# Optimization experiments

Hardware: AMD Instinct MI355X
Metric: run time of the kernel (lower is better)

Reference implementation:

```python
import jax, jax.numpy as jnp
import numpy as np

INPUT_DIM = 512
HIDDEN_DIM = 512
T, B = 512, 128


def setup_inputs() -> dict:
    key = jax.random.key(0)
    ks = jax.random.split(key, 9)
    s_in = 1.0 / np.sqrt(INPUT_DIM + HIDDEN_DIM)
    d = INPUT_DIM + HIDDEN_DIM
    inputs = jax.random.normal(ks[0], (T, B, INPUT_DIM), dtype=jnp.float32)
    def lin(kw, kb):
        W = jax.random.uniform(kw, (HIDDEN_DIM, d), minval=-s_in, maxval=s_in, dtype=jnp.float32)
        b = jax.random.uniform(kb, (HIDDEN_DIM,), minval=-s_in, maxval=s_in, dtype=jnp.float32)
        return W, b
    Wf, bf = lin(ks[1], ks[2])
    Wi, bi = lin(ks[3], ks[4])
    Wg, bg = lin(ks[5], ks[6])
    Wo, bo = lin(ks[7], ks[8])
    return {"inputs": inputs, "Wf": Wf, "bf": bf, "Wi": Wi, "bi": bi,
            "Wg": Wg, "bg": bg, "Wo": Wo, "bo": bo}


def _lstm(inputs, Wf, bf, Wi, bi, Wg, bg, Wo, bo):
    B_ = inputs.shape[1]
    h0 = jnp.zeros((B_, HIDDEN_DIM), dtype=inputs.dtype)
    c0 = jnp.zeros((B_, HIDDEN_DIM), dtype=inputs.dtype)

    def step(carry, x):
        hx, cx = carry
        combined = jnp.concatenate([x, hx], axis=1)  # [B, input+hidden]
        f = jax.nn.sigmoid(combined @ Wf.T + bf)
        i = jax.nn.sigmoid(combined @ Wi.T + bi)
        g = jnp.tanh(combined @ Wg.T + bg)
        o = jax.nn.sigmoid(combined @ Wo.T + bo)
        cx = f * cx + i * g
        hx = o * jnp.tanh(cx)
        return (hx, cx), hx

    (hx, cx), outputs = jax.lax.scan(step, (h0, c0), inputs)
    return outputs, (hx, cx)


def reference(inputs, Wf, bf, Wi, bi, Wg, bg, Wo, bo):
    return _lstm(inputs, Wf, bf, Wi, bi, Wg, bg, Wo, bo)
```

## Files before the change

kernel.cpp:

```cpp
#include <hip/hip_runtime.h>
#include <stdint.h>

#define T_STEPS 512
#define BATCH   128
#define HID     512
#define KTOT    1024

typedef __attribute__((ext_vector_type(8))) short          bf16x8;
typedef __attribute__((ext_vector_type(8))) unsigned short u16x8;
typedef __attribute__((ext_vector_type(4))) float          f32x4;

__device__ inline unsigned short f2bf(float f) {
    union { float f; unsigned u; } x; x.f = f;
    unsigned r = x.u + 0x7FFFu + ((x.u >> 16) & 1u);
    return (unsigned short)(r >> 16);
}

__device__ inline float sigmoidf_(float x) { return 1.f / (1.f + __expf(-x)); }
__device__ inline float tanhf_(float x)    { float e = __expf(2.f * x); return 1.f - 2.f / (e + 1.f); }

__global__ void cast_x_kernel(const float* __restrict__ x, unsigned short* __restrict__ y, int n) {
    int i = (blockIdx.x * blockDim.x + threadIdx.x) * 8;
    if (i >= n) return;
    float4 a = *(const float4*)(x + i);
    float4 b = *(const float4*)(x + i + 4);
    u16x8 v;
    v[0] = f2bf(a.x); v[1] = f2bf(a.y); v[2] = f2bf(a.z); v[3] = f2bf(a.w);
    v[4] = f2bf(b.x); v[5] = f2bf(b.y); v[6] = f2bf(b.z); v[7] = f2bf(b.w);
    *(u16x8*)(y + i) = v;
}

__global__ __launch_bounds__(512, 2) void lstm_kernel(
    const float* __restrict__ xf,
    const unsigned short* __restrict__ xbf,
    const float* __restrict__ Wf, const float* __restrict__ bfv,
    const float* __restrict__ Wi, const float* __restrict__ biv,
    const float* __restrict__ Wg, const float* __restrict__ bgv,
    const float* __restrict__ Wo, const float* __restrict__ bov,
    float* __restrict__ out,
    unsigned int* __restrict__ flags,
    unsigned short* __restrict__ hbuf,
    int use_xbf)
{
    __shared__ __align__(16) unsigned short comb[16][1048];
    __shared__ float gatesl[4][16][33];
    __shared__ float cl[16][33];

    const int tid  = threadIdx.x;
    const int bgc  = blockIdx.x >> 4;
    const int cg   = blockIdx.x & 15;
    const int w    = tid >> 6;
    const int lane = tid & 63;
    const int gate = w & 3;
    const int uh   = w >> 2;
    const int n    = lane & 15;
    const int quad = lane >> 4;
    const int unit = cg * 32 + uh * 16 + n;

    const float* Wp = (gate == 0) ? Wf : (gate == 1) ? Wi : (gate == 2) ? Wg : Wo;
    const float* bp = (gate == 0) ? bfv : (gate == 1) ? biv : (gate == 2) ? bgv : bov;
    const float bias = bp[unit];

    bf16x8 wfr[32];
    const float* wrow = Wp + (size_t)unit * KTOT;
#pragma unroll
    for (int kk = 0; kk < 32; ++kk) {
        const float4* p = (const float4*)(wrow + kk * 32 + quad * 8);
        float4 a = p[0], b = p[1];
        u16x8 v;
        v[0] = f2bf(a.x); v[1] = f2bf(a.y); v[2] = f2bf(a.z); v[3] = f2bf(a.w);
        v[4] = f2bf(b.x); v[5] = f2bf(b.y); v[6] = f2bf(b.z); v[7] = f2bf(b.w);
        wfr[kk] = (bf16x8)v;
    }

    {
        const int b = tid >> 5, u = tid & 31;
        cl[b][u] = 0.f;
    }

    const int srow = tid >> 5;
    const int scol = tid & 31;

    for (int t = 0; t < T_STEPS; ++t) {
        if (use_xbf) {
            const uint4* src = (const uint4*)(xbf + ((size_t)(t * BATCH + bgc * 16 + srow)) * HID + scol * 16);
            uint4 v0 = src[0], v1 = src[1];
            *(uint4*)&comb[srow][scol * 16]     = v0;
            *(uint4*)&comb[srow][scol * 16 + 8] = v1;
        } else {
            const float4* src = (const float4*)(xf + ((size_t)(t * BATCH + bgc * 16 + srow)) * HID + scol * 16);
            float4 a0 = src[0], a1 = src[1], a2 = src[2], a3 = src[3];
            u16x8 v;
            v[0] = f2bf(a0.x); v[1] = f2bf(a0.y); v[2] = f2bf(a0.z); v[3] = f2bf(a0.w);
            v[4] = f2bf(a1.x); v[5] = f2bf(a1.y); v[6] = f2bf(a1.z); v[7] = f2bf(a1.w);
            *(u16x8*)&comb[srow][scol * 16] = v;
            u16x8 v2;
            v2[0] = f2bf(a2.x); v2[1] = f2bf(a2.y); v2[2] = f2bf(a2.z); v2[3] = f2bf(a2.w);
            v2[4] = f2bf(a3.x); v2[5] = f2bf(a3.y); v2[6] = f2bf(a3.z); v2[7] = f2bf(a3.w);
            *(u16x8*)&comb[srow][scol * 16 + 8] = v2;
        }
        __syncthreads();

        f32x4 acc0a = {0.f, 0.f, 0.f, 0.f}, acc0b = {0.f, 0.f, 0.f, 0.f};
#pragma unroll
        for (int kk = 0; kk < 16; kk += 2) {
            bf16x8 a0 = *(const bf16x8*)&comb[n][kk * 32 + quad * 8];
            bf16x8 a1 = *(const bf16x8*)&comb[n][(kk + 1) * 32 + quad * 8];
            acc0a = __builtin_amdgcn_mfma_f32_16x16x32_bf16(a0, wfr[kk],     acc0a, 0, 0, 0);
            acc0b = __builtin_amdgcn_mfma_f32_16x16x32_bf16(a1, wfr[kk + 1], acc0b, 0, 0, 0);
        }

        if (t > 0) {
            if (tid < 16) {
                unsigned int* fp = flags + ((size_t)(t - 1) * 8 + bgc) * 16 + tid;
                while (__hip_atomic_load(fp, __ATOMIC_RELAXED, __HIP_MEMORY_SCOPE_AGENT) == 0u) {
                    __builtin_amdgcn_s_sleep(1);
                }
            }
            __syncthreads();
            const unsigned long long* src = (const unsigned long long*)
                (hbuf + (size_t)((t - 1) & 1) * BATCH * HID + (size_t)(bgc * 16 + srow) * HID + scol * 16);
            unsigned long long v0 = __hip_atomic_load(src + 0, __ATOMIC_RELAXED, __HIP_MEMORY_SCOPE_AGENT);
            unsigned long long v1 = __hip_atomic_load(src + 1, __ATOMIC_RELAXED, __HIP_MEMORY_SCOPE_AGENT);
            unsigned long long v2 = __hip_atomic_load(src + 2, __ATOMIC_RELAXED, __HIP_MEMORY_SCOPE_AGENT);
            unsigned long long v3 = __hip_atomic_load(src + 3, __ATOMIC_RELAXED, __HIP_MEMORY_SCOPE_AGENT);
            unsigned long long* dst = (unsigned long long*)&comb[srow][512 + scol * 16];
            dst[0] = v0; dst[1] = v1; dst[2] = v2; dst[3] = v3;
        } else {
            uint4 z = {0u, 0u, 0u, 0u};
            *(uint4*)&comb[srow][512 + scol * 16]     = z;
            *(uint4*)&comb[srow][512 + scol * 16 + 8] = z;
        }
        __syncthreads();

        f32x4 acc1a = {0.f, 0.f, 0.f, 0.f}, acc1b = {0.f, 0.f, 0.f, 0.f};
#pragma unroll
        for (int kk = 16; kk < 32; kk += 2) {
            bf16x8 a0 = *(const bf16x8*)&comb[n][kk * 32 + quad * 8];
            bf16x8 a1 = *(const bf16x8*)&comb[n][(kk + 1) * 32 + quad * 8];
            acc1a = __builtin_amdgcn_mfma_f32_16x16x32_bf16(a0, wfr[kk],     acc1a, 0, 0, 0);
            acc1b = __builtin_amdgcn_mfma_f32_16x16x32_bf16(a1, wfr[kk + 1], acc1b, 0, 0, 0);
        }

#pragma unroll
        for (int r = 0; r < 4; ++r) {
            float v = acc0a[r] + acc0b[r] + acc1a[r] + acc1b[r] + bias;
            v = (gate == 2) ? tanhf_(v) : sigmoidf_(v);
            gatesl[gate][quad * 4 + r][uh * 16 + n] = v;
        }
        __syncthreads();

        {
            const int b = tid >> 5, u = tid & 31;
            float fv = gatesl[0][b][u], iv = gatesl[1][b][u];
            float gv = gatesl[2][b][u], ov = gatesl[3][b][u];
            float cn = fv * cl[b][u] + iv * gv;
            cl[b][u] = cn;
            float hv = ov * tanhf_(cn);
            const int bglob = bgc * 16 + b;
            const int uglob = cg * 32 + u;
            out[(size_t)t * BATCH * HID + (size_t)bglob * HID + uglob] = hv;
            if (t == T_STEPS - 1) {
                out[(size_t)T_STEPS * BATCH * HID + (size_t)bglob * HID + uglob] = hv;
                out[(size_t)T_STEPS * BATCH * HID + BATCH * HID + (size_t)bglob * HID + uglob] = cn;
            }
            unsigned int us  = (unsigned int)f2bf(hv);
            unsigned int us1 = (unsigned int)__shfl_down((int)us, 1);
            if ((u & 1) == 0) {
                unsigned int pv = us | (us1 << 16);
                unsigned int* hp = (unsigned int*)(hbuf + (size_t)(t & 1) * BATCH * HID
                                                   + (size_t)bglob * HID + uglob);
                __hip_atomic_store(hp, pv, __ATOMIC_RELAXED, __HIP_MEMORY_SCOPE_AGENT);
            }
        }
        __builtin_amdgcn_s_waitcnt(0);
        __syncthreads();
        if (tid == 0) {
            __hip_atomic_store(flags + ((size_t)t * 8 + bgc) * 16 + cg, 1u,
                               __ATOMIC_RELAXED, __HIP_MEMORY_SCOPE_AGENT);
        }
    }
}

extern "C" void kernel_launch(void* const* d_in, const int* in_sizes, int n_in,
                              void* d_out, int out_size, void* d_ws, size_t ws_size,
                              hipStream_t stream) {
    (void)in_sizes; (void)n_in; (void)out_size;
    const float* x   = (const float*)d_in[0];
    const float* Wf  = (const float*)d_in[1];
    const float* bfv = (const float*)d_in[2];
    const float* Wi  = (const float*)d_in[3];
    const float* biv = (const float*)d_in[4];
    const float* Wg  = (const float*)d_in[5];
    const float* bgv = (const float*)d_in[6];
    const float* Wo  = (const float*)d_in[7];
    const float* bov = (const float*)d_in[8];
    float* out = (float*)d_out;

    unsigned char* ws = (unsigned char*)d_ws;
    unsigned int*   flags = (unsigned int*)ws;
    unsigned short* hbuf  = (unsigned short*)(ws + 262144);
    unsigned short* xbf   = (unsigned short*)(ws + 524288);

    size_t need = 524288 + (size_t)T_STEPS * BATCH * HID * 2;
    int use_xbf = (ws_size >= need) ? 1 : 0;

    hipMemsetAsync(flags, 0, 262144, stream);
    if (use_xbf) {
        int nelem = T_STEPS * BATCH * HID;
        cast_x_kernel<<<nelem / (256 * 8), 256, 0, stream>>>(x, xbf, nelem);
    }
    lstm_kernel<<<dim3(128), dim3(512), 0, stream>>>(
        x, xbf, Wf, bfv, Wi, biv, Wg, bgv, Wo, bov, out, flags, hbuf, use_xbf);
}
```

Before: 1.971 ms.

## Software-pipeline input projection and prefetch x ahead of the recurrent wait

Restructures the time loop so the input half of the gate GEMM for step t+1 is computed right after step t's gate math. The next x tile is prefetched two steps ahead into registers and written to shared memory early, so global load latency and the x-part MFMAs sit off the wait for the hidden state. The cell state moves from shared memory into a per-thread register. Every wave now spins on the flags itself without sleeping, which removes one block barrier but adds polling traffic. The x-part MFMAs now run before the step's completion flag is published, which may lengthen the cross-block critical path.

```diff
diff --git a/kernel.cpp b/kernel.cpp
--- a/kernel.cpp
+++ b/kernel.cpp
@@ -28,6 +28,25 @@
     v[0] = f2bf(a.x); v[1] = f2bf(a.y); v[2] = f2bf(a.z); v[3] = f2bf(a.w);
     v[4] = f2bf(b.x); v[5] = f2bf(b.y); v[6] = f2bf(b.z); v[7] = f2bf(b.w);
     *(u16x8*)(y + i) = v;
+}
+
+__device__ inline void load_x32(const float* xf, const unsigned short* xbf, int use_xbf,
+                                size_t off, uint4& a, uint4& b) {
+    if (use_xbf) {
+        const uint4* p = (const uint4*)(xbf + off);
+        a = p[0]; b = p[1];
+    } else {
+        const float4* p = (const float4*)(xf + off);
+        float4 f0 = p[0], f1 = p[1], f2 = p[2], f3 = p[3];
+        u16x8 v;
+        v[0] = f2bf(f0.x); v[1] = f2bf(f0.y); v[2] = f2bf(f0.z); v[3] = f2bf(f0.w);
+        v[4] = f2bf(f1.x); v[5] = f2bf(f1.y); v[6] = f2bf(f1.z); v[7] = f2bf(f1.w);
+        a = *(uint4*)&v;
+        u16x8 w;
+        w[0] = f2bf(f2.x); w[1] = f2bf(f2.y); w[2] = f2bf(f2.z); w[3] = f2bf(f2.w);
+        w[4] = f2bf(f3.x); w[5] = f2bf(f3.y); w[6] = f2bf(f3.z); w[7] = f2bf(f3.w);
+        b = *(uint4*)&w;
+    }
 }
 
 __global__ __launch_bounds__(512, 2) void lstm_kernel(
@@ -44,7 +63,6 @@
 {
     __shared__ __align__(16) unsigned short comb[16][1048];
     __shared__ float gatesl[4][16][33];
-    __shared__ float cl[16][33];
 
     const int tid  = threadIdx.x;
     const int bgc  = blockIdx.x >> 4;
@@ -73,111 +91,123 @@
         wfr[kk] = (bf16x8)v;
     }
 
-    {
-        const int b = tid >> 5, u = tid & 31;
-        cl[b][u] = 0.f;
-    }
-
     const int srow = tid >> 5;
     const int scol = tid & 31;
 
+    const int bc = srow, uc = scol;
+    float creg = 0.f;
+    const int bglob = bgc * 16 + bc;
+    const int uglob = cg * 32 + uc;
+
+    const size_t xstride = (size_t)HID;
+
+    {
+        uint4 a, b;
+        load_x32(xf, xbf, use_xbf, ((size_t)(0 * BATCH + bgc * 16 + srow)) * xstride + scol * 16, a, b);
+        *(uint4*)&comb[srow][scol * 16]     = a;
+        *(uint4*)&comb[srow][scol * 16 + 8] = b;
+        uint4 z = {0u, 0u, 0u, 0u};
+        *(uint4*)&comb[srow][512 + scol * 16]     = z;
+        *(uint4*)&comb[srow][512 + scol * 16 + 8] = z;
+    }
+    __syncthreads();
+
+    f32x4 axa = {0.f, 0.f, 0.f, 0.f}, axb = {0.f, 0.f, 0.f, 0.f};
+#pragma unroll
+    for (int kk = 0; kk < 16; kk += 2) {
+        bf16x8 a0 = *(const bf16x8*)&comb[n][kk * 32 + quad * 8];
+        bf16x8 a1 = *(const bf16x8*)&comb[n][(kk + 1) * 32 + quad * 8];
+        axa = __builtin_amdgcn_mfma_f32_16x16x32_bf16(a0, wfr[kk],     axa, 0, 0, 0);
+        axb = __builtin_amdgcn_mfma_f32_16x16x32_bf16(a1, wfr[kk + 1], axb, 0, 0, 0);
+    }
+
+    uint4 pfa, pfb;
+    load_x32(xf, xbf, use_xbf, ((size_t)(1 * BATCH + bgc * 16 + srow)) * xstride + scol * 16, pfa, pfb);
+
     for (int t = 0; t < T_STEPS; ++t) {
-        if (use_xbf) {
-            const uint4* src = (const uint4*)(xbf + ((size_t)(t * BATCH + bgc * 16 + srow)) * HID + scol * 16);
-            uint4 v0 = src[0], v1 = src[1];
-            *(uint4*)&comb[srow][scol * 16]     = v0;
-            *(uint4*)&comb[srow][scol * 16 + 8] = v1;
-        } else {
-            const float4* src = (const float4*)(xf + ((size_t)(t * BATCH + bgc * 16 + srow)) * HID + scol * 16);
-            float4 a0 = src[0], a1 = src[1], a2 = src[2], a3 = src[3];
-            u16x8 v;
-            v[0] = f2bf(a0.x); v[1] = f2bf(a0.y); v[2] = f2bf(a0.z); v[3] = f2bf(a0.w);
-            v[4] = f2bf(a1.x); v[5] = f2bf(a1.y); v[6] = f2bf(a1.z); v[7] = f2bf(a1.w);
-            *(u16x8*)&comb[srow][scol * 16] = v;
-            u16x8 v2;
-            v2[0] = f2bf(a2.x); v2[1] = f2bf(a2.y); v2[2] = f2bf(a2.z); v2[3] = f2bf(a2.w);
-            v2[4] = f2bf(a3.x); v2[5] = f2bf(a3.y); v2[6] = f2bf(a3.z); v2[7] = f2bf(a3.w);
-            *(u16x8*)&comb[srow][scol * 16 + 8] = v2;
-        }
-        __syncthreads();
-
-        f32x4 acc0a = {0.f, 0.f, 0.f, 0.f}, acc0b = {0.f, 0.f, 0.f, 0.f};
-#pragma unroll
-        for (int kk = 0; kk < 16; kk += 2) {
-            bf16x8 a0 = *(const bf16x8*)&comb[n][kk * 32 + quad * 8];
-            bf16x8 a1 = *(const bf16x8*)&comb[n][(kk + 1) * 32 + quad * 8];
-            acc0a = __builtin_amdgcn_mfma_f32_16x16x32_bf16(a0, wfr[kk],     acc0a, 0, 0, 0);
-            acc0b = __builtin_amdgcn_mfma_f32_16x16x32_bf16(a1, wfr[kk + 1], acc0b, 0, 0, 0);
-        }
-
         if (t > 0) {
-            if (tid < 16) {
-                unsigned int* fp = flags + ((size_t)(t - 1) * 8 + bgc) * 16 + tid;
-                while (__hip_atomic_load(fp, __ATOMIC_RELAXED, __HIP_MEMORY_SCOPE_AGENT) == 0u) {
-                    __builtin_amdgcn_s_sleep(1);
-                }
-            }
-            __syncthreads();
+            if (lane < 16) {
+                unsigned int* fp = flags + ((size_t)(t - 1) * 8 + bgc) * 16 + lane;
+                while (__hip_atomic_load(fp, __ATOMIC_RELAXED, __HIP_MEMORY_SCOPE_AGENT) == 0u) {}
+            }
             const unsigned long long* src = (const unsigned long long*)
                 (hbuf + (size_t)((t - 1) & 1) * BATCH * HID + (size_t)(bgc * 16 + srow) * HID + scol * 16);
             unsigned long long v0 = __hip_atomic_load(src + 0, __ATOMIC_RELAXED, __HIP_MEMORY_SCOPE_AGENT);
             unsigned long long v1 = __hip_atomic_load(src + 1, __ATOMIC_RELAXED, __HIP_MEMORY_SCOPE_AGENT);
             unsigned long long v2 = __hip_atomic_load(src + 2, __ATOMIC_RELAXED, __HIP_MEMORY_SCOPE_AGENT);
             unsigned long long v3 = __hip_atomic_load(src + 3, __ATOMIC_RELAXED, __HIP_MEMORY_SCOPE_AGENT);
-            unsigned long long* dst = (unsigned long long*)&comb[srow][512 + scol * 16];
-            dst[0] = v0; dst[1] = v1; dst[2] = v2; dst[3] = v3;
-        } else {
-            uint4 z = {0u, 0u, 0u, 0u};
-            *(uint4*)&comb[srow][512 + scol * 16]     = z;
-            *(uint4*)&comb[srow][512 + scol * 16 + 8] = z;
+            uint4 a, b;
+            a.x = (unsigned)v0; a.y = (unsigned)(v0 >> 32);
+            a.z = (unsigned)v1; a.w = (unsigned)(v1 >> 32);
+            b.x = (unsigned)v2; b.y = (unsigned)(v2 >> 32);
+            b.z = (unsigned)v3; b.w = (unsigned)(v3 >> 32);
+            *(uint4*)&comb[srow][512 + scol * 16]     = a;
+            *(uint4*)&comb[srow][512 + scol * 16 + 8] = b;
         }
         __syncthreads();
 
-        f32x4 acc1a = {0.f, 0.f, 0.f, 0.f}, acc1b = {0.f, 0.f, 0.f, 0.f};
 #pragma unroll
         for (int kk = 16; kk < 32; kk += 2) {
             bf16x8 a0 = *(const bf16x8*)&comb[n][kk * 32 + quad * 8];
             bf16x8 a1 = *(const bf16x8*)&comb[n][(kk + 1) * 32 + quad * 8];
-            acc1a = __builtin_amdgcn_mfma_f32_16x16x32_bf16(a0, wfr[kk],     acc1a, 0, 0, 0);
-            acc1b = __builtin_amdgcn_mfma_f32_16x16x32_bf16(a1, wfr[kk + 1], acc1b, 0, 0, 0);
+            axa = __builtin_amdgcn_mfma_f32_16x16x32_bf16(a0, wfr[kk],     axa, 0, 0, 0);
+            axb = __builtin_amdgcn_mfma_f32_16x16x32_bf16(a1, wfr[kk + 1], axb, 0, 0, 0);
         }
 
 #pragma unroll
         for (int r = 0; r < 4; ++r) {
-            float v = acc0a[r] + acc0b[r] + acc1a[r] + acc1b[r] + bias;
+            float v = axa[r] + axb[r] + bias;
             v = (gate == 2) ? tanhf_(v) : sigmoidf_(v);
             gatesl[gate][quad * 4 + r][uh * 16 + n] = v;
         }
+        if (t + 1 < T_STEPS) {
+            *(uint4*)&comb[srow][scol * 16]     = pfa;
+            *(uint4*)&comb[srow][scol * 16 + 8] = pfb;
+        }
         __syncthreads();
 
         {
-            const int b = tid >> 5, u = tid & 31;
-            float fv = gatesl[0][b][u], iv = gatesl[1][b][u];
-            float gv = gatesl[2][b][u], ov = gatesl[3][b][u];
-            float cn = fv * cl[b][u] + iv * gv;
-            cl[b][u] = cn;
+            float fv = gatesl[0][bc][uc], iv = gatesl[1][bc][uc];
+            float gv = gatesl[2][bc][uc], ov = gatesl[3][bc][uc];
+            float cn = fv * creg + iv * gv;
+            creg = cn;
             float hv = ov * tanhf_(cn);
-            const int bglob = bgc * 16 + b;
-            const int uglob = cg * 32 + u;
+            unsigned int us  = (unsigned int)f2bf(hv);
+            unsigned int us1 = (unsigned int)__shfl_down((int)us, 1);
+            if ((uc & 1) == 0) {
+                unsigned int pv = us | (us1 << 16);
+                unsigned int* hp = (unsigned int*)(hbuf + (size_t)(t & 1) * BATCH * HID
+                                                   + (size_t)bglob * HID + uglob);
+                __hip_atomic_store(hp, pv, __ATOMIC_RELAXED, __HIP_MEMORY_SCOPE_AGENT);
+            }
             out[(size_t)t * BATCH * HID + (size_t)bglob * HID + uglob] = hv;
             if (t == T_STEPS - 1) {
                 out[(size_t)T_STEPS * BATCH * HID + (size_t)bglob * HID + uglob] = hv;
                 out[(size_t)T_STEPS * BATCH * HID + BATCH * HID + (size_t)bglob * HID + uglob] = cn;
             }
-            unsigned int us  = (unsigned int)f2bf(hv);
-            unsigned int us1 = (unsigned int)__shfl_down((int)us, 1);
-            if ((u & 1) == 0) {
-                unsigned int pv = us | (us1 << 16);
-                unsigned int* hp = (unsigned int*)(hbuf + (size_t)(t & 1) * BATCH * HID
-                                                   + (size_t)bglob * HID + uglob);
-                __hip_atomic_store(hp, pv, __ATOMIC_RELAXED, __HIP_MEMORY_SCOPE_AGENT);
-            }
-        }
+        }
+
+        if (t + 1 < T_STEPS) {
+            axa = (f32x4){0.f, 0.f, 0.f, 0.f};
+            axb = (f32x4){0.f, 0.f, 0.f, 0.f};
+#pragma unroll
+            for (int kk = 0; kk < 16; kk += 2) {
+                bf16x8 a0 = *(const bf16x8*)&comb[n][kk * 32 + quad * 8];
+                bf16x8 a1 = *(const bf16x8*)&comb[n][(kk + 1) * 32 + quad * 8];
+                axa = __builtin_amdgcn_mfma_f32_16x16x32_bf16(a0, wfr[kk],     axa, 0, 0, 0);
+                axb = __builtin_amdgcn_mfma_f32_16x16x32_bf16(a1, wfr[kk + 1], axb, 0, 0, 0);
+            }
+        }
+
         __builtin_amdgcn_s_waitcnt(0);
         __syncthreads();
         if (tid == 0) {
             __hip_atomic_store(flags + ((size_t)t * 8 + bgc) * 16 + cg, 1u,
                                __ATOMIC_RELAXED, __HIP_MEMORY_SCOPE_AGENT);
+        }
+        if (t + 2 < T_STEPS) {
+            load_x32(xf, xbf, use_xbf,
+                     ((size_t)((t + 2) * BATCH + bgc * 16 + srow)) * xstride + scol * 16, pfa, pfb);
         }
     }
 }
```

New measurement: 1.936 ms. No clear change (-1.7%).
